# Performance work log

Hardware: AMD Instinct MI355X
Metric: run time of the kernel (lower is better)

Reference implementation:

```python
import jax, jax.numpy as jnp
import numpy as np
from jax import lax
from jax.scipy.special import logsumexp

B, T, H, L = 64, 512, 768, 9


def setup_inputs() -> dict:
    key = jax.random.key(0)
    k1, k2, k3, k4, k5 = jax.random.split(key, 5)
    hidden = jax.random.normal(k1, (B, T, H), dtype=jnp.float32)
    W = jax.random.normal(k2, (L, H), dtype=jnp.float32) * 0.02
    b = jnp.zeros((L,), dtype=jnp.float32)
    transitions = jax.random.normal(k3, (L, L), dtype=jnp.float32) * 0.1
    lengths = jax.random.randint(k4, (B,), T // 2, T + 1)
    seq_mask = jnp.arange(T)[None, :] < lengths[:, None]          # [B,T] bool
    labels = jax.random.randint(k5, (B, T), 0, L).astype(jnp.int32)
    labels = jnp.where(seq_mask, labels, -100).astype(jnp.int32)   # -100 = ignore
    attention_mask = seq_mask.astype(jnp.int32)
    return {"hidden": hidden, "W": W, "b": b, "transitions": transitions,
            "labels": labels, "attention_mask": attention_mask}


def _crf_nll(logits, tags, transitions, mask):
    # numerator: joint score of the gold path (no start/end transitions)
    maskf = mask.astype(logits.dtype)
    emit = jnp.take_along_axis(logits, tags[..., None], axis=2)[..., 0]   # [B,T]
    emit_score = (emit * maskf).sum(-1)
    trans = transitions[tags[:, :-1], tags[:, 1:]]                        # [B,T-1]
    trans_score = (trans * maskf[:, 1:]).sum(-1)
    numerator = emit_score + trans_score
    # denominator: forward algorithm (log-sum-exp recurrence over time)
    def step(alpha, xs):
        logit_t, mask_t = xs                                   # [B,L], [B]
        inner = alpha[:, :, None] + transitions[None, :, :] + logit_t[:, None, :]
        new = logsumexp(inner, axis=1)
        return jnp.where(mask_t[:, None], new, alpha), None
    alpha0 = logits[:, 0]                                      # mask[:,0] assumed True
    alpha, _ = lax.scan(step, alpha0,
                        (jnp.transpose(logits[:, 1:], (1, 0, 2)), mask[:, 1:].T))
    denominator = logsumexp(alpha, axis=-1)
    return -(numerator - denominator).sum()


def _viterbi(logits, transitions, mask):
    num_tags = transitions.shape[0]
    identity_bp = jnp.broadcast_to(jnp.arange(num_tags)[None, :], logits.shape[:1] + (num_tags,))

    def vstep(vscore, xs):
        logit_t, mask_t = xs
        inner = vscore[:, :, None] + transitions[None, :, :]   # [B,L_prev,L_cur]
        bp = jnp.argmax(inner, axis=1)                         # [B,L]
        new = jnp.max(inner, axis=1) + logit_t
        vscore = jnp.where(mask_t[:, None], new, vscore)
        bp = jnp.where(mask_t[:, None], bp, identity_bp)       # carry tag through pad
        return vscore, bp

    vscore0 = logits[:, 0]
    vscore, bps = lax.scan(vstep, vscore0,
                           (jnp.transpose(logits[:, 1:], (1, 0, 2)), mask[:, 1:].T))
    last_tag = jnp.argmax(vscore, axis=-1)                     # [B]

    def btstep(tag, bp_t):
        prev = jnp.take_along_axis(bp_t, tag[:, None], axis=1)[:, 0]
        return prev, tag

    first_tag, tags_rest = lax.scan(btstep, last_tag, bps, reverse=True)  # ys[t]=tag_{t+1}
    return jnp.concatenate([first_tag[:, None], tags_rest.T], axis=1)     # [B,T]


def reference(hidden, W, b, transitions, labels, attention_mask):
    mask = (attention_mask != 0) & (labels != -100)            # create_combined_mask
    logits = jnp.einsum('bth,lh->btl', hidden, W) + b          # classifier (dropout=eval)
    tags = jnp.where(labels == -100, 0, labels)                # adjust_labels_for_crf
    loss = _crf_nll(logits, tags, transitions, mask)           # -log_likelihood (summed)
    vtags = _viterbi(logits, transitions, mask)                # [B,T]
    # pad_predictions: prepend -100, shift right, -100 outside the masked span
    bsz = hidden.shape[0]
    neg = jnp.full((bsz, 1), -100, dtype=jnp.int32)
    shifted = jnp.concatenate([neg, vtags[:, :-1].astype(jnp.int32)], axis=1)
    valid = jnp.concatenate([jnp.zeros((bsz, 1), bool), mask[:, :-1]], axis=1)
    predictions = jnp.where(valid, shifted, -100)
    return loss, predictions
```

## Files before the change

### kernel.cpp

```cpp
#include <hip/hip_runtime.h>

#define BATCH 64
#define TLEN  512
#define HDIM  768
#define LTAGS 9

#define WS_LOGD 0
#define WS_LOGF 2359296
#define WS_VM   3538944
#define WS_AM   6193152
#define WS_NUM  6856704
#define WS_LOSS 6857216

__global__ __launch_bounds__(256) void logits_kernel(
    const float* __restrict__ hidden, const float* __restrict__ W,
    const float* __restrict__ bvec, double* __restrict__ logitsD,
    float* __restrict__ logitsF)
{
    __shared__ float sW[LTAGS * HDIM];
    __shared__ float sb[LTAGS];
    const int tid = threadIdx.x;
    for (int i = tid; i < LTAGS * HDIM; i += 256) sW[i] = W[i];
    if (tid < LTAGS) sb[tid] = bvec[tid];
    __syncthreads();

    const int lane = tid & 63;
    const int wave = tid >> 6;
    const int sub  = lane & 7;
    const int rg   = lane >> 3;

    const int rowBase = blockIdx.x * 64 + wave * 16;
    const int r0 = rowBase + rg;
    const int r1 = rowBase + rg + 8;
    const float* h0p = hidden + (size_t)r0 * HDIM;
    const float* h1p = hidden + (size_t)r1 * HDIM;

    double acc0[LTAGS], acc1[LTAGS];
    #pragma unroll
    for (int l = 0; l < LTAGS; ++l) { acc0[l] = 0.0; acc1[l] = 0.0; }

    #pragma unroll 2
    for (int i = 0; i < 24; ++i) {
        const int off = i * 32 + sub * 4;
        const float4 h0 = *(const float4*)(h0p + off);
        const float4 h1 = *(const float4*)(h1p + off);
        #pragma unroll
        for (int l = 0; l < LTAGS; ++l) {
            const float4 w = *(const float4*)&sW[l * HDIM + off];
            float d0 = h0.x * w.x;
            d0 = fmaf(h0.y, w.y, d0); d0 = fmaf(h0.z, w.z, d0); d0 = fmaf(h0.w, w.w, d0);
            float d1 = h1.x * w.x;
            d1 = fmaf(h1.y, w.y, d1); d1 = fmaf(h1.z, w.z, d1); d1 = fmaf(h1.w, w.w, d1);
            acc0[l] += (double)d0;
            acc1[l] += (double)d1;
        }
    }
    #pragma unroll
    for (int l = 0; l < LTAGS; ++l) {
        double v0 = acc0[l], v1 = acc1[l];
        #pragma unroll
        for (int off = 4; off > 0; off >>= 1) {
            v0 += __shfl_down(v0, off);
            v1 += __shfl_down(v1, off);
        }
        acc0[l] = v0; acc1[l] = v1;
    }
    if (sub == 0) {
        #pragma unroll
        for (int l = 0; l < LTAGS; ++l) {
            double v0 = acc0[l] + (double)sb[l];
            double v1 = acc1[l] + (double)sb[l];
            logitsD[(size_t)r0 * LTAGS + l] = v0;
            logitsD[(size_t)r1 * LTAGS + l] = v1;
            logitsF[(size_t)r0 * LTAGS + l] = (float)v0;
            logitsF[(size_t)r1 * LTAGS + l] = (float)v1;
        }
    }
}

__global__ __launch_bounds__(256) void chunk_kernel(
    const float* __restrict__ trans, const int* __restrict__ labels,
    const int* __restrict__ att, const double* __restrict__ logitsD,
    const float* __restrict__ logitsF,
    double* __restrict__ wsVM, float* __restrict__ wsAM,
    double* __restrict__ wsNum)
{
    __shared__ double sT64[81];
    __shared__ float  sE32[81];
    const int tid = threadIdx.x;
    if (tid < 81) { float tv = trans[tid]; sT64[tid] = (double)tv; sE32[tid] = __expf(tv); }
    __syncthreads();

    const int blk = blockIdx.x;
    if (blk < 144) {
        const int gid = blk * 256 + tid;
        const int b   = gid / 576;
        const int rem = gid - b * 576;
        const int c   = rem / 9;
        const int i   = rem - c * 9;

        double M[LTAGS];
        #pragma unroll
        for (int j = 0; j < LTAGS; ++j) M[j] = (i == j) ? 0.0 : -1e300;

        const double* lrow = logitsD + ((size_t)b * TLEN + (c * 8 + 1)) * LTAGS;
        const int* lab = labels + b * TLEN;
        const int* am  = att + b * TLEN;
        const int t0 = c * 8 + 1;

        double lg[LTAGS], lgN[LTAGS];
        #pragma unroll
        for (int j = 0; j < LTAGS; ++j) lg[j] = lrow[j];
        bool mk = (am[t0] != 0) && (lab[t0] != -100);

        for (int s = 0; s < 8; ++s) {
            bool mkN = false;
            const int tn = t0 + s + 1;
            if (s < 7 && tn <= TLEN - 1) {
                const double* ln = lrow + (s + 1) * LTAGS;
                #pragma unroll
                for (int j = 0; j < LTAGS; ++j) lgN[j] = ln[j];
                mkN = (am[tn] != 0) && (lab[tn] != -100);
            }
            double nw[LTAGS];
            #pragma unroll
            for (int j = 0; j < LTAGS; ++j) {
                double bst = M[0] + sT64[j];
                #pragma unroll
                for (int k = 1; k < LTAGS; ++k) {
                    double cnd = M[k] + sT64[k * LTAGS + j];
                    bst = fmax(bst, cnd);
                }
                nw[j] = bst + lg[j];
            }
            #pragma unroll
            for (int j = 0; j < LTAGS; ++j) { M[j] = mk ? nw[j] : M[j]; lg[j] = lgN[j]; }
            mk = mkN;
        }
        double* dst = wsVM + (((size_t)b * 64 + c) * LTAGS + i) * LTAGS;
        #pragma unroll
        for (int j = 0; j < LTAGS; ++j) dst[j] = M[j];
    } else if (blk < 216) {
        const int gid = (blk - 144) * 256 + tid;
        const int b   = gid / 288;
        const int rem = gid - b * 288;
        const int c   = rem / 9;
        const int i   = rem - c * 9;

        float M[LTAGS];
        #pragma unroll
        for (int j = 0; j < LTAGS; ++j) M[j] = (i == j) ? 0.f : -1e30f;

        const float* lrow = logitsF + ((size_t)b * TLEN + (c * 16 + 1)) * LTAGS;
        const int* lab = labels + b * TLEN;
        const int* am  = att + b * TLEN;
        const int t0 = c * 16 + 1;

        float lg[LTAGS], lgN[LTAGS];
        #pragma unroll
        for (int j = 0; j < LTAGS; ++j) lg[j] = lrow[j];
        bool mk = (am[t0] != 0) && (lab[t0] != -100);

        for (int s = 0; s < 16; ++s) {
            bool mkN = false;
            const int tn = t0 + s + 1;
            if (s < 15 && tn <= TLEN - 1) {
                const float* ln = lrow + (s + 1) * LTAGS;
                #pragma unroll
                for (int j = 0; j < LTAGS; ++j) lgN[j] = ln[j];
                mkN = (am[tn] != 0) && (lab[tn] != -100);
            }
            float m = M[0];
            #pragma unroll
            for (int k = 1; k < LTAGS; ++k) m = fmaxf(m, M[k]);
            float P[LTAGS];
            #pragma unroll
            for (int k = 0; k < LTAGS; ++k) P[k] = __expf(M[k] - m);
            float nw[LTAGS];
            #pragma unroll
            for (int j = 0; j < LTAGS; ++j) {
                float sacc = P[0] * sE32[j];
                #pragma unroll
                for (int k = 1; k < LTAGS; ++k) sacc = fmaf(P[k], sE32[k * LTAGS + j], sacc);
                nw[j] = m + __logf(sacc) + lg[j];
            }
            #pragma unroll
            for (int j = 0; j < LTAGS; ++j) { M[j] = mk ? nw[j] : M[j]; lg[j] = lgN[j]; }
            mk = mkN;
        }
        float* dst = wsAM + (((size_t)b * 32 + c) * LTAGS + i) * LTAGS;
        #pragma unroll
        for (int j = 0; j < LTAGS; ++j) dst[j] = M[j];
    } else {
        const int bb   = (blk - 216) * 4 + (tid >> 6);
        const int lane = tid & 63;
        const int* lab = labels + bb * TLEN;
        const int* am  = att + bb * TLEN;
        const double* lrowb = logitsD + (size_t)bb * TLEN * LTAGS;
        double part = 0.0;
        #pragma unroll
        for (int k = 0; k < 8; ++k) {
            const int t = lane + k * 64;
            int lv = lab[t], av = am[t];
            bool mkc = (av != 0) && (lv != -100);
            int tg = (lv == -100) ? 0 : lv;
            if (mkc) part += lrowb[(size_t)t * LTAGS + tg];
            if (t < TLEN - 1) {
                int lv2 = lab[t + 1], av2 = am[t + 1];
                bool mk2 = (av2 != 0) && (lv2 != -100);
                int tg2 = (lv2 == -100) ? 0 : lv2;
                if (mk2) part += sT64[tg * LTAGS + tg2];
            }
        }
        #pragma unroll
        for (int off = 32; off > 0; off >>= 1) part += __shfl_down(part, off);
        if (lane == 0) wsNum[bb] = part;
    }
}

__global__ __launch_bounds__(128) void crf2_kernel(
    const float* __restrict__ trans, const int* __restrict__ labels,
    const int* __restrict__ att, const double* __restrict__ logitsD,
    const double* __restrict__ wsVM, const float* __restrict__ wsAM,
    const double* __restrict__ wsNum, double* __restrict__ wsLoss,
    float* __restrict__ out)
{
    __shared__ __align__(16) double sVM[64 * 81];
    __shared__ __align__(16) float  sAM[32 * 81];
    __shared__ double sVstart[65 * LTAGS];
    __shared__ unsigned long long sBPp[513];
    __shared__ int sTagB[65];
    __shared__ double sT64[81];
    __shared__ unsigned char sMk[513];
    __shared__ double sDen;
    __shared__ int sLast;

    const int b = blockIdx.x, tid = threadIdx.x;
    const int wave = tid >> 6, lane = tid & 63;
    const unsigned long long IDMAP = 0x876543210ull;

    const double2* gVM = (const double2*)(wsVM + (size_t)b * 64 * 81);
    double2* sVM2 = (double2*)sVM;
    for (int i = tid; i < 2592; i += 128) sVM2[i] = gVM[i];
    const float4* gAM = (const float4*)(wsAM + (size_t)b * 32 * 81);
    float4* sAM4 = (float4*)sAM;
    for (int i = tid; i < 648; i += 128) sAM4[i] = gAM[i];

    const int* lab = labels + b * TLEN;
    const int* am  = att + b * TLEN;
    for (int t = tid; t < TLEN; t += 128) {
        int lv = lab[t], av = am[t];
        sMk[t] = (av != 0 && lv != -100) ? 1 : 0;
    }
    if (tid == 0) sMk[TLEN] = 0;
    if (tid < 81) sT64[tid] = (double)trans[tid];
    __syncthreads();

    if (wave == 0) {
        const int j = (lane < LTAGS) ? lane : (LTAGS - 1);
        double v = logitsD[(size_t)b * TLEN * LTAGS + j];
        double Mc[LTAGS], Mn[LTAGS];
        #pragma unroll
        for (int i = 0; i < LTAGS; ++i) Mc[i] = sVM[i * LTAGS + j];
        for (int c = 0; c < 64; ++c) {
            if (c < 63) {
                #pragma unroll
                for (int i = 0; i < LTAGS; ++i) Mn[i] = sVM[(c + 1) * 81 + i * LTAGS + j];
            }
            if (lane < LTAGS) sVstart[c * LTAGS + j] = v;
            double g[LTAGS];
            #pragma unroll
            for (int i = 0; i < LTAGS; ++i) g[i] = __shfl(v, i);
            double bst = g[0] + Mc[0];
            #pragma unroll
            for (int i = 1; i < LTAGS; ++i) bst = fmax(bst, g[i] + Mc[i]);
            v = bst;
            if (c < 63) {
                #pragma unroll
                for (int i = 0; i < LTAGS; ++i) Mc[i] = Mn[i];
            }
        }
        if (lane < LTAGS) sVstart[64 * LTAGS + j] = v;
        double g[LTAGS];
        #pragma unroll
        for (int i = 0; i < LTAGS; ++i) g[i] = __shfl(v, i);
        if (lane == 0) {
            int bi = 0; double bv = g[0];
            #pragma unroll
            for (int i = 1; i < LTAGS; ++i) if (g[i] > bv) { bv = g[i]; bi = i; }
            sLast = bi;
        }
    } else {
        const int j = (lane < LTAGS) ? lane : (LTAGS - 1);
        float v = (float)logitsD[(size_t)b * TLEN * LTAGS + j];
        float Mc[LTAGS], Mn[LTAGS];
        #pragma unroll
        for (int i = 0; i < LTAGS; ++i) Mc[i] = sAM[i * LTAGS + j];
        for (int c = 0; c < 32; ++c) {
            if (c < 31) {
                #pragma unroll
                for (int i = 0; i < LTAGS; ++i) Mn[i] = sAM[(c + 1) * 81 + i * LTAGS + j];
            }
            float g[LTAGS];
            #pragma unroll
            for (int i = 0; i < LTAGS; ++i) g[i] = __shfl(v, i);
            float a[LTAGS];
            #pragma unroll
            for (int i = 0; i < LTAGS; ++i) a[i] = g[i] + Mc[i];
            float m = a[0];
            #pragma unroll
            for (int i = 1; i < LTAGS; ++i) m = fmaxf(m, a[i]);
            float sacc = 0.f;
            #pragma unroll
            for (int i = 0; i < LTAGS; ++i) sacc += __expf(a[i] - m);
            v = m + __logf(sacc);
            if (c < 31) {
                #pragma unroll
                for (int i = 0; i < LTAGS; ++i) Mc[i] = Mn[i];
            }
        }
        float g[LTAGS];
        #pragma unroll
        for (int i = 0; i < LTAGS; ++i) g[i] = __shfl(v, i);
        if (lane == 0) {
            float m = g[0];
            #pragma unroll
            for (int i = 1; i < LTAGS; ++i) m = fmaxf(m, g[i]);
            float sacc = 0.f;
            #pragma unroll
            for (int i = 0; i < LTAGS; ++i) sacc += __expf(g[i] - m);
            sDen = (double)(m + __logf(sacc));
        }
    }
    __syncthreads();

    unsigned long long S = IDMAP;
    if (tid < 64) {
        const int c = tid;
        double v[LTAGS];
        #pragma unroll
        for (int j = 0; j < LTAGS; ++j) v[j] = sVstart[c * LTAGS + j];
        const double* lrow = logitsD + ((size_t)b * TLEN + (c * 8 + 1)) * LTAGS;
        double lg[LTAGS], lgN[LTAGS];
        #pragma unroll
        for (int j = 0; j < LTAGS; ++j) lg[j] = lrow[j];

        for (int s = 0; s < 8; ++s) {
            const int t = c * 8 + 1 + s;
            if (s < 7 && t + 1 <= TLEN - 1) {
                const double* ln = lrow + (s + 1) * LTAGS;
                #pragma unroll
                for (int j = 0; j < LTAGS; ++j) lgN[j] = ln[j];
            }
            const bool mk = (sMk[t] != 0);
            unsigned long long pk = 0;
            double nv[LTAGS];
            #pragma unroll
            for (int j = 0; j < LTAGS; ++j) {
                double bst = v[0] + sT64[j];
                int bi = 0;
                #pragma unroll
                for (int k = 1; k < LTAGS; ++k) {
                    double cnd = v[k] + sT64[k * LTAGS + j];
                    bool gt = cnd > bst;
                    bst = gt ? cnd : bst;
                    bi  = gt ? k : bi;
                }
                nv[j] = bst + lg[j];
                pk |= ((unsigned long long)bi) << (4 * j);
            }
            pk = mk ? pk : IDMAP;
            sBPp[t] = pk;
            #pragma unroll
            for (int j = 0; j < LTAGS; ++j) { v[j] = mk ? nv[j] : v[j]; lg[j] = lgN[j]; }
        }
        unsigned long long G = IDMAP;
        for (int s = 7; s >= 0; --s) {
            const unsigned long long bp = sBPp[c * 8 + 1 + s];
            unsigned long long ng = 0;
            #pragma unroll
            for (int j = 0; j < LTAGS; ++j) {
                int gj = (int)((G >> (4 * j)) & 15);
                int f  = (int)((bp >> (4 * gj)) & 15);
                ng |= ((unsigned long long)f) << (4 * j);
            }
            G = ng;
        }
        S = G;
    }

    #pragma unroll
    for (int d = 1; d < 64; d <<= 1) {
        unsigned long long Sn = __shfl_down(S, d);
        if (wave == 0 && lane + d < 64) {
            unsigned long long R = 0;
            #pragma unroll
            for (int x = 0; x < LTAGS; ++x) {
                int y = (int)((Sn >> (4 * x)) & 15);
                int z = (int)((S >> (4 * y)) & 15);
                R |= ((unsigned long long)z) << (4 * x);
            }
            S = R;
        }
    }
    if (tid < 64) {
        const int lt = sLast;
        sTagB[tid] = (int)((S >> (4 * lt)) & 15);
        if (tid == 0) sTagB[64] = lt;
    }
    __syncthreads();

    if (tid < 64) {
        const int c = tid;
        int cur = sTagB[c + 1];
        float* po = out + 1 + b * TLEN;
        for (int s = 8; s >= 1; --s) {
            const int t = c * 8 + s;
            if (t < TLEN) {
                int nxt = (int)((sBPp[t] >> (4 * cur)) & 15);
                po[t] = sMk[t - 1] ? (float)nxt : -100.f;
                cur = nxt;
            }
        }
    }
    if (tid == 0) {
        out[1 + b * TLEN] = -100.f;
        wsLoss[b] = sDen - wsNum[b];
    }
}

__global__ __launch_bounds__(64) void loss_kernel(
    const double* __restrict__ wsLoss, float* __restrict__ out)
{
    double v = wsLoss[threadIdx.x];
    #pragma unroll
    for (int off = 32; off > 0; off >>= 1) v += __shfl_down(v, off);
    if (threadIdx.x == 0) out[0] = (float)v;
}

extern "C" void kernel_launch(void* const* d_in, const int* in_sizes, int n_in,
                              void* d_out, int out_size, void* d_ws, size_t ws_size,
                              hipStream_t stream)
{
    const float* hidden = (const float*)d_in[0];
    const float* W      = (const float*)d_in[1];
    const float* bvec   = (const float*)d_in[2];
    const float* trans  = (const float*)d_in[3];
    const int*   labels = (const int*)d_in[4];
    const int*   att    = (const int*)d_in[5];
    float* out = (float*)d_out;

    char* ws = (char*)d_ws;
    double* logitsD = (double*)(ws + WS_LOGD);
    float*  logitsF = (float*)(ws + WS_LOGF);
    double* wsVM    = (double*)(ws + WS_VM);
    float*  wsAM    = (float*)(ws + WS_AM);
    double* wsNum   = (double*)(ws + WS_NUM);
    double* wsLoss  = (double*)(ws + WS_LOSS);

    logits_kernel<<<512, 256, 0, stream>>>(hidden, W, bvec, logitsD, logitsF);
    chunk_kernel<<<232, 256, 0, stream>>>(trans, labels, att, logitsD, logitsF,
                                          wsVM, wsAM, wsNum);
    crf2_kernel<<<BATCH, 128, 0, stream>>>(trans, labels, att, logitsD,
                                           wsVM, wsAM, wsNum, wsLoss, out);
    loss_kernel<<<1, 64, 0, stream>>>(wsLoss, out);
}
```

Measured before the change: 218.6 us.

## Fuse CRF chunk, combine, and loss kernels into one split-block kernel

Merges the chunked max-plus/log-sum-exp matrix kernel, the per-batch combine kernel and the loss reduction into one 128-block kernel. Viterbi and forward-algorithm work for each sequence go to separate blocks, chunk matrices stay in shared memory instead of global workspace, and the last block to finish sums the loss through an atomic ticket. The Viterbi backpointer pass now spreads across 9 lanes per chunk using shuffles, and backpointers are stored as bytes. This removes two kernel launches and the global round trips, at the cost of larger 576-thread blocks, heavier shared memory use, and only 128 blocks to fill the GPU.

```diff
diff --git a/kernel.cpp b/kernel.cpp
--- a/kernel.cpp
+++ b/kernel.cpp
@@ -7,19 +7,18 @@
 
 #define WS_LOGD 0
 #define WS_LOGF 2359296
-#define WS_VM   3538944
-#define WS_AM   6193152
-#define WS_NUM  6856704
-#define WS_LOSS 6857216
+#define WS_LOSS 3538944
+#define WS_CNT  3539456
 
 __global__ __launch_bounds__(256) void logits_kernel(
     const float* __restrict__ hidden, const float* __restrict__ W,
     const float* __restrict__ bvec, double* __restrict__ logitsD,
-    float* __restrict__ logitsF)
+    float* __restrict__ logitsF, unsigned int* __restrict__ wsCnt)
 {
     __shared__ float sW[LTAGS * HDIM];
     __shared__ float sb[LTAGS];
     const int tid = threadIdx.x;
+    if (blockIdx.x == 0 && tid == 0) *wsCnt = 0u;
     for (int i = tid; i < LTAGS * HDIM; i += 256) sW[i] = W[i];
     if (tid < LTAGS) sb[tid] = bvec[tid];
     __syncthreads();
@@ -78,364 +77,333 @@
     }
 }
 
-__global__ __launch_bounds__(256) void chunk_kernel(
+__global__ __launch_bounds__(576) void crf_fused(
     const float* __restrict__ trans, const int* __restrict__ labels,
     const int* __restrict__ att, const double* __restrict__ logitsD,
-    const float* __restrict__ logitsF,
-    double* __restrict__ wsVM, float* __restrict__ wsAM,
-    double* __restrict__ wsNum)
-{
-    __shared__ double sT64[81];
-    __shared__ float  sE32[81];
-    const int tid = threadIdx.x;
-    if (tid < 81) { float tv = trans[tid]; sT64[tid] = (double)tv; sE32[tid] = __expf(tv); }
-    __syncthreads();
-
-    const int blk = blockIdx.x;
-    if (blk < 144) {
-        const int gid = blk * 256 + tid;
-        const int b   = gid / 576;
-        const int rem = gid - b * 576;
-        const int c   = rem / 9;
-        const int i   = rem - c * 9;
-
-        double M[LTAGS];
-        #pragma unroll
-        for (int j = 0; j < LTAGS; ++j) M[j] = (i == j) ? 0.0 : -1e300;
-
-        const double* lrow = logitsD + ((size_t)b * TLEN + (c * 8 + 1)) * LTAGS;
-        const int* lab = labels + b * TLEN;
-        const int* am  = att + b * TLEN;
-        const int t0 = c * 8 + 1;
-
-        double lg[LTAGS], lgN[LTAGS];
-        #pragma unroll
-        for (int j = 0; j < LTAGS; ++j) lg[j] = lrow[j];
-        bool mk = (am[t0] != 0) && (lab[t0] != -100);
-
-        for (int s = 0; s < 8; ++s) {
-            bool mkN = false;
-            const int tn = t0 + s + 1;
-            if (s < 7 && tn <= TLEN - 1) {
-                const double* ln = lrow + (s + 1) * LTAGS;
-                #pragma unroll
-                for (int j = 0; j < LTAGS; ++j) lgN[j] = ln[j];
-                mkN = (am[tn] != 0) && (lab[tn] != -100);
-            }
-            double nw[LTAGS];
-            #pragma unroll
-            for (int j = 0; j < LTAGS; ++j) {
-                double bst = M[0] + sT64[j];
-                #pragma unroll
-                for (int k = 1; k < LTAGS; ++k) {
-                    double cnd = M[k] + sT64[k * LTAGS + j];
-                    bst = fmax(bst, cnd);
-                }
-                nw[j] = bst + lg[j];
-            }
-            #pragma unroll
-            for (int j = 0; j < LTAGS; ++j) { M[j] = mk ? nw[j] : M[j]; lg[j] = lgN[j]; }
-            mk = mkN;
-        }
-        double* dst = wsVM + (((size_t)b * 64 + c) * LTAGS + i) * LTAGS;
-        #pragma unroll
-        for (int j = 0; j < LTAGS; ++j) dst[j] = M[j];
-    } else if (blk < 216) {
-        const int gid = (blk - 144) * 256 + tid;
-        const int b   = gid / 288;
-        const int rem = gid - b * 288;
-        const int c   = rem / 9;
-        const int i   = rem - c * 9;
-
-        float M[LTAGS];
-        #pragma unroll
-        for (int j = 0; j < LTAGS; ++j) M[j] = (i == j) ? 0.f : -1e30f;
-
-        const float* lrow = logitsF + ((size_t)b * TLEN + (c * 16 + 1)) * LTAGS;
-        const int* lab = labels + b * TLEN;
-        const int* am  = att + b * TLEN;
-        const int t0 = c * 16 + 1;
-
-        float lg[LTAGS], lgN[LTAGS];
-        #pragma unroll
-        for (int j = 0; j < LTAGS; ++j) lg[j] = lrow[j];
-        bool mk = (am[t0] != 0) && (lab[t0] != -100);
-
-        for (int s = 0; s < 16; ++s) {
-            bool mkN = false;
-            const int tn = t0 + s + 1;
-            if (s < 15 && tn <= TLEN - 1) {
-                const float* ln = lrow + (s + 1) * LTAGS;
-                #pragma unroll
-                for (int j = 0; j < LTAGS; ++j) lgN[j] = ln[j];
-                mkN = (am[tn] != 0) && (lab[tn] != -100);
-            }
-            float m = M[0];
-            #pragma unroll
-            for (int k = 1; k < LTAGS; ++k) m = fmaxf(m, M[k]);
-            float P[LTAGS];
-            #pragma unroll
-            for (int k = 0; k < LTAGS; ++k) P[k] = __expf(M[k] - m);
-            float nw[LTAGS];
-            #pragma unroll
-            for (int j = 0; j < LTAGS; ++j) {
-                float sacc = P[0] * sE32[j];
-                #pragma unroll
-                for (int k = 1; k < LTAGS; ++k) sacc = fmaf(P[k], sE32[k * LTAGS + j], sacc);
-                nw[j] = m + __logf(sacc) + lg[j];
-            }
-            #pragma unroll
-            for (int j = 0; j < LTAGS; ++j) { M[j] = mk ? nw[j] : M[j]; lg[j] = lgN[j]; }
-            mk = mkN;
-        }
-        float* dst = wsAM + (((size_t)b * 32 + c) * LTAGS + i) * LTAGS;
-        #pragma unroll
-        for (int j = 0; j < LTAGS; ++j) dst[j] = M[j];
-    } else {
-        const int bb   = (blk - 216) * 4 + (tid >> 6);
-        const int lane = tid & 63;
-        const int* lab = labels + bb * TLEN;
-        const int* am  = att + bb * TLEN;
-        const double* lrowb = logitsD + (size_t)bb * TLEN * LTAGS;
-        double part = 0.0;
-        #pragma unroll
-        for (int k = 0; k < 8; ++k) {
-            const int t = lane + k * 64;
-            int lv = lab[t], av = am[t];
-            bool mkc = (av != 0) && (lv != -100);
-            int tg = (lv == -100) ? 0 : lv;
-            if (mkc) part += lrowb[(size_t)t * LTAGS + tg];
-            if (t < TLEN - 1) {
-                int lv2 = lab[t + 1], av2 = am[t + 1];
-                bool mk2 = (av2 != 0) && (lv2 != -100);
-                int tg2 = (lv2 == -100) ? 0 : lv2;
-                if (mk2) part += sT64[tg * LTAGS + tg2];
-            }
-        }
-        #pragma unroll
-        for (int off = 32; off > 0; off >>= 1) part += __shfl_down(part, off);
-        if (lane == 0) wsNum[bb] = part;
-    }
-}
-
-__global__ __launch_bounds__(128) void crf2_kernel(
-    const float* __restrict__ trans, const int* __restrict__ labels,
-    const int* __restrict__ att, const double* __restrict__ logitsD,
-    const double* __restrict__ wsVM, const float* __restrict__ wsAM,
-    const double* __restrict__ wsNum, double* __restrict__ wsLoss,
-    float* __restrict__ out)
+    const float* __restrict__ logitsF, double* __restrict__ wsLoss,
+    unsigned int* __restrict__ wsCnt, float* __restrict__ out)
 {
     __shared__ __align__(16) double sVM[64 * 81];
     __shared__ __align__(16) float  sAM[32 * 81];
     __shared__ double sVstart[65 * LTAGS];
-    __shared__ unsigned long long sBPp[513];
+    __shared__ unsigned char sBPb[513 * 16];
+    __shared__ double sT64[81];
+    __shared__ float  sE32[81];
+    __shared__ unsigned char sMk[TLEN + 1];
     __shared__ int sTagB[65];
-    __shared__ double sT64[81];
-    __shared__ unsigned char sMk[513];
-    __shared__ double sDen;
+    __shared__ double sDen, sNum;
     __shared__ int sLast;
-
-    const int b = blockIdx.x, tid = threadIdx.x;
+    __shared__ unsigned int sTicket;
+
+    const int tid  = threadIdx.x;
     const int wave = tid >> 6, lane = tid & 63;
-    const unsigned long long IDMAP = 0x876543210ull;
-
-    const double2* gVM = (const double2*)(wsVM + (size_t)b * 64 * 81);
-    double2* sVM2 = (double2*)sVM;
-    for (int i = tid; i < 2592; i += 128) sVM2[i] = gVM[i];
-    const float4* gAM = (const float4*)(wsAM + (size_t)b * 32 * 81);
-    float4* sAM4 = (float4*)sAM;
-    for (int i = tid; i < 648; i += 128) sAM4[i] = gAM[i];
-
+    const int blk  = blockIdx.x;
+    const bool isVit = (blk < BATCH);
+    const int b = isVit ? blk : (blk - BATCH);
+
+    if (tid < 81) { float tv = trans[tid]; sT64[tid] = (double)tv; sE32[tid] = __expf(tv); }
     const int* lab = labels + b * TLEN;
     const int* am  = att + b * TLEN;
-    for (int t = tid; t < TLEN; t += 128) {
-        int lv = lab[t], av = am[t];
-        sMk[t] = (av != 0 && lv != -100) ? 1 : 0;
+    for (int t = tid; t < TLEN; t += 576)
+        sMk[t] = (am[t] != 0 && lab[t] != -100) ? 1 : 0;
+    if (tid == 0) sMk[TLEN] = 0;
+    __syncthreads();
+
+    if (isVit) {
+        {
+            const int c = tid / 9;
+            const int i = tid - c * 9;
+            double M[LTAGS];
+            #pragma unroll
+            for (int j = 0; j < LTAGS; ++j) M[j] = (i == j) ? 0.0 : -1e300;
+
+            const double* lrow = logitsD + ((size_t)b * TLEN + (c * 8 + 1)) * LTAGS;
+            const int t0 = c * 8 + 1;
+            double lg[LTAGS], lgN[LTAGS];
+            #pragma unroll
+            for (int j = 0; j < LTAGS; ++j) lg[j] = lrow[j];
+            bool mk = sMk[t0] != 0;
+
+            for (int s = 0; s < 8; ++s) {
+                bool mkN = false;
+                const int tn = t0 + s + 1;
+                if (s < 7 && tn <= TLEN - 1) {
+                    const double* ln = lrow + (s + 1) * LTAGS;
+                    #pragma unroll
+                    for (int j = 0; j < LTAGS; ++j) lgN[j] = ln[j];
+                    mkN = sMk[tn] != 0;
+                }
+                double nw[LTAGS];
+                #pragma unroll
+                for (int j = 0; j < LTAGS; ++j) {
+                    double bst = M[0] + sT64[j];
+                    #pragma unroll
+                    for (int k = 1; k < LTAGS; ++k) {
+                        double cnd = M[k] + sT64[k * LTAGS + j];
+                        bst = fmax(bst, cnd);
+                    }
+                    nw[j] = bst + lg[j];
+                }
+                #pragma unroll
+                for (int j = 0; j < LTAGS; ++j) { M[j] = mk ? nw[j] : M[j]; lg[j] = lgN[j]; }
+                mk = mkN;
+            }
+            double* dst = &sVM[(c * LTAGS + i) * LTAGS];
+            #pragma unroll
+            for (int j = 0; j < LTAGS; ++j) dst[j] = M[j];
+        }
+        __syncthreads();
+
+        if (wave == 0) {
+            const int j = (lane < LTAGS) ? lane : (LTAGS - 1);
+            double v = logitsD[(size_t)b * TLEN * LTAGS + j];
+            double Mc[LTAGS], Mn[LTAGS];
+            #pragma unroll
+            for (int i = 0; i < LTAGS; ++i) Mc[i] = sVM[i * LTAGS + j];
+            for (int c = 0; c < 64; ++c) {
+                if (c < 63) {
+                    #pragma unroll
+                    for (int i = 0; i < LTAGS; ++i) Mn[i] = sVM[(c + 1) * 81 + i * LTAGS + j];
+                }
+                if (lane < LTAGS) sVstart[c * LTAGS + j] = v;
+                double g[LTAGS];
+                #pragma unroll
+                for (int i = 0; i < LTAGS; ++i) g[i] = __shfl(v, i);
+                double bst = g[0] + Mc[0];
+                #pragma unroll
+                for (int i = 1; i < LTAGS; ++i) bst = fmax(bst, g[i] + Mc[i]);
+                v = bst;
+                if (c < 63) {
+                    #pragma unroll
+                    for (int i = 0; i < LTAGS; ++i) Mc[i] = Mn[i];
+                }
+            }
+            if (lane < LTAGS) sVstart[64 * LTAGS + j] = v;
+            double g[LTAGS];
+            #pragma unroll
+            for (int i = 0; i < LTAGS; ++i) g[i] = __shfl(v, i);
+            if (lane == 0) {
+                int bi = 0; double bv = g[0];
+                #pragma unroll
+                for (int i = 1; i < LTAGS; ++i) if (g[i] > bv) { bv = g[i]; bi = i; }
+                sLast = bi;
+            }
+        }
+        __syncthreads();
+
+        {
+            const int grp = tid >> 4;
+            const int lig = tid & 15;
+            const int jr = (lig < 9) ? lig : 8;
+            const int gbase = lane & 48;
+            for (int pass = 0; pass < 2; ++pass) {
+                const int c = pass * 36 + grp;
+                if (c < 64) {
+                    double v = sVstart[c * LTAGS + jr];
+                    const double* lrow = logitsD + ((size_t)b * TLEN + (c * 8 + 1)) * LTAGS;
+                    double lg = lrow[jr];
+                    for (int s = 0; s < 8; ++s) {
+                        const int t = c * 8 + 1 + s;
+                        double lgN = 0.0;
+                        if (s < 7 && t + 1 <= TLEN - 1) lgN = lrow[(s + 1) * LTAGS + jr];
+                        const bool mk = sMk[t] != 0;
+                        double g0 = __shfl(v, gbase + 0);
+                        double bst = g0 + sT64[jr];
+                        int bi = 0;
+                        #pragma unroll
+                        for (int k = 1; k < LTAGS; ++k) {
+                            double gk = __shfl(v, gbase + k);
+                            double cnd = gk + sT64[k * LTAGS + jr];
+                            bool gt = cnd > bst;
+                            bst = gt ? cnd : bst;
+                            bi  = gt ? k : bi;
+                        }
+                        double nv = bst + lg;
+                        int bp = mk ? bi : jr;
+                        if (lig < 9) sBPb[t * 16 + lig] = (unsigned char)bp;
+                        v  = mk ? nv : v;
+                        lg = lgN;
+                    }
+                }
+            }
+        }
+        __syncthreads();
+
+        if (tid < 64) {
+            int Gm[LTAGS];
+            #pragma unroll
+            for (int j = 0; j < LTAGS; ++j) Gm[j] = j;
+            for (int s = 7; s >= 0; --s) {
+                const int t = tid * 8 + 1 + s;
+                #pragma unroll
+                for (int j = 0; j < LTAGS; ++j) Gm[j] = sBPb[t * 16 + Gm[j]];
+            }
+            unsigned long long S = 0;
+            #pragma unroll
+            for (int j = 0; j < LTAGS; ++j) S |= ((unsigned long long)Gm[j]) << (4 * j);
+
+            #pragma unroll
+            for (int d = 1; d < 64; d <<= 1) {
+                unsigned long long Sn = __shfl_down(S, d);
+                if (lane + d < 64) {
+                    unsigned long long R = 0;
+                    #pragma unroll
+                    for (int x = 0; x < LTAGS; ++x) {
+                        int y = (int)((Sn >> (4 * x)) & 15);
+                        int z = (int)((S >> (4 * y)) & 15);
+                        R |= ((unsigned long long)z) << (4 * x);
+                    }
+                    S = R;
+                }
+            }
+            const int lt = sLast;
+            sTagB[tid] = (int)((S >> (4 * lt)) & 15);
+            if (tid == 0) sTagB[64] = lt;
+        }
+        __syncthreads();
+
+        if (tid < 64) {
+            const int c = tid;
+            int cur = sTagB[c + 1];
+            float* po = out + 1 + b * TLEN;
+            for (int s = 8; s >= 1; --s) {
+                const int t = c * 8 + s;
+                if (t < TLEN) {
+                    int nxt = (int)sBPb[t * 16 + cur];
+                    po[t] = sMk[t - 1] ? (float)nxt : -100.f;
+                    cur = nxt;
+                }
+            }
+        }
+        if (tid == 0) out[1 + b * TLEN] = -100.f;
+    } else {
+        if (tid < 288) {
+            const int c = tid / 9;
+            const int i = tid - c * 9;
+            float M[LTAGS];
+            #pragma unroll
+            for (int j = 0; j < LTAGS; ++j) M[j] = (i == j) ? 0.f : -1e30f;
+
+            const float* lrow = logitsF + ((size_t)b * TLEN + (c * 16 + 1)) * LTAGS;
+            const int t0 = c * 16 + 1;
+            float lg[LTAGS], lgN[LTAGS];
+            #pragma unroll
+            for (int j = 0; j < LTAGS; ++j) lg[j] = lrow[j];
+            bool mk = sMk[t0] != 0;
+
+            for (int s = 0; s < 16; ++s) {
+                bool mkN = false;
+                const int tn = t0 + s + 1;
+                if (s < 15 && tn <= TLEN - 1) {
+                    const float* ln = lrow + (s + 1) * LTAGS;
+                    #pragma unroll
+                    for (int j = 0; j < LTAGS; ++j) lgN[j] = ln[j];
+                    mkN = sMk[tn] != 0;
+                }
+                float m = M[0];
+                #pragma unroll
+                for (int k = 1; k < LTAGS; ++k) m = fmaxf(m, M[k]);
+                float P[LTAGS];
+                #pragma unroll
+                for (int k = 0; k < LTAGS; ++k) P[k] = __expf(M[k] - m);
+                float nw[LTAGS];
+                #pragma unroll
+                for (int j = 0; j < LTAGS; ++j) {
+                    float sacc = P[0] * sE32[j];
+                    #pragma unroll
+                    for (int k = 1; k < LTAGS; ++k) sacc = fmaf(P[k], sE32[k * LTAGS + j], sacc);
+                    nw[j] = m + __logf(sacc) + lg[j];
+                }
+                #pragma unroll
+                for (int j = 0; j < LTAGS; ++j) { M[j] = mk ? nw[j] : M[j]; lg[j] = lgN[j]; }
+                mk = mkN;
+            }
+            float* dst = &sAM[(c * LTAGS + i) * LTAGS];
+            #pragma unroll
+            for (int j = 0; j < LTAGS; ++j) dst[j] = M[j];
+        } else if (tid >= 512) {
+            const double* lrowb = logitsD + (size_t)b * TLEN * LTAGS;
+            double part = 0.0;
+            #pragma unroll
+            for (int k = 0; k < 8; ++k) {
+                const int t = lane + k * 64;
+                int lv = lab[t], av = am[t];
+                bool mkc = (av != 0) && (lv != -100);
+                int tg = (lv == -100) ? 0 : lv;
+                if (mkc) part += lrowb[(size_t)t * LTAGS + tg];
+                if (t < TLEN - 1) {
+                    int lv2 = lab[t + 1], av2 = am[t + 1];
+                    bool mk2 = (av2 != 0) && (lv2 != -100);
+                    int tg2 = (lv2 == -100) ? 0 : lv2;
+                    if (mk2) part += sT64[tg * LTAGS + tg2];
+                }
+            }
+            #pragma unroll
+            for (int off = 32; off > 0; off >>= 1) part += __shfl_down(part, off);
+            if (lane == 0) sNum = part;
+        }
+        __syncthreads();
+
+        if (wave == 0) {
+            const int j = (lane < LTAGS) ? lane : (LTAGS - 1);
+            float v = (float)logitsD[(size_t)b * TLEN * LTAGS + j];
+            float Mc[LTAGS], Mn[LTAGS];
+            #pragma unroll
+            for (int i = 0; i < LTAGS; ++i) Mc[i] = sAM[i * LTAGS + j];
+            for (int c = 0; c < 32; ++c) {
+                if (c < 31) {
+                    #pragma unroll
+                    for (int i = 0; i < LTAGS; ++i) Mn[i] = sAM[(c + 1) * 81 + i * LTAGS + j];
+                }
+                float g[LTAGS];
+                #pragma unroll
+                for (int i = 0; i < LTAGS; ++i) g[i] = __shfl(v, i);
+                float a[LTAGS];
+                #pragma unroll
+                for (int i = 0; i < LTAGS; ++i) a[i] = g[i] + Mc[i];
+                float m = a[0];
+                #pragma unroll
+                for (int i = 1; i < LTAGS; ++i) m = fmaxf(m, a[i]);
+                float sacc = 0.f;
+                #pragma unroll
+                for (int i = 0; i < LTAGS; ++i) sacc += __expf(a[i] - m);
+                v = m + __logf(sacc);
+                if (c < 31) {
+                    #pragma unroll
+                    for (int i = 0; i < LTAGS; ++i) Mc[i] = Mn[i];
+                }
+            }
+            float g[LTAGS];
+            #pragma unroll
+            for (int i = 0; i < LTAGS; ++i) g[i] = __shfl(v, i);
+            if (lane == 0) {
+                float m = g[0];
+                #pragma unroll
+                for (int i = 1; i < LTAGS; ++i) m = fmaxf(m, g[i]);
+                float sacc = 0.f;
+                #pragma unroll
+                for (int i = 0; i < LTAGS; ++i) sacc += __expf(g[i] - m);
+                sDen = (double)(m + __logf(sacc));
+            }
+        }
+        __syncthreads();
+
+        if (tid == 0) {
+            wsLoss[b] = sDen - sNum;
+            __threadfence();
+            sTicket = atomicAdd(wsCnt, 1u);
+        }
+        __syncthreads();
+        if (sTicket == (BATCH - 1)) {
+            __threadfence();
+            if (tid < 64) {
+                double v = wsLoss[tid];
+                #pragma unroll
+                for (int off = 32; off > 0; off >>= 1) v += __shfl_down(v, off);
+                if (tid == 0) out[0] = (float)v;
+            }
+        }
     }
-    if (tid == 0) sMk[TLEN] = 0;
-    if (tid < 81) sT64[tid] = (double)trans[tid];
-    __syncthreads();
-
-    if (wave == 0) {
-        const int j = (lane < LTAGS) ? lane : (LTAGS - 1);
-        double v = logitsD[(size_t)b * TLEN * LTAGS + j];
-        double Mc[LTAGS], Mn[LTAGS];
-        #pragma unroll
-        for (int i = 0; i < LTAGS; ++i) Mc[i] = sVM[i * LTAGS + j];
-        for (int c = 0; c < 64; ++c) {
-            if (c < 63) {
-                #pragma unroll
-                for (int i = 0; i < LTAGS; ++i) Mn[i] = sVM[(c + 1) * 81 + i * LTAGS + j];
-            }
-            if (lane < LTAGS) sVstart[c * LTAGS + j] = v;
-            double g[LTAGS];
-            #pragma unroll
-            for (int i = 0; i < LTAGS; ++i) g[i] = __shfl(v, i);
-            double bst = g[0] + Mc[0];
-            #pragma unroll
-            for (int i = 1; i < LTAGS; ++i) bst = fmax(bst, g[i] + Mc[i]);
-            v = bst;
-            if (c < 63) {
-                #pragma unroll
-                for (int i = 0; i < LTAGS; ++i) Mc[i] = Mn[i];
-            }
-        }
-        if (lane < LTAGS) sVstart[64 * LTAGS + j] = v;
-        double g[LTAGS];
-        #pragma unroll
-        for (int i = 0; i < LTAGS; ++i) g[i] = __shfl(v, i);
-        if (lane == 0) {
-            int bi = 0; double bv = g[0];
-            #pragma unroll
-            for (int i = 1; i < LTAGS; ++i) if (g[i] > bv) { bv = g[i]; bi = i; }
-            sLast = bi;
-        }
-    } else {
-        const int j = (lane < LTAGS) ? lane : (LTAGS - 1);
-        float v = (float)logitsD[(size_t)b * TLEN * LTAGS + j];
-        float Mc[LTAGS], Mn[LTAGS];
-        #pragma unroll
-        for (int i = 0; i < LTAGS; ++i) Mc[i] = sAM[i * LTAGS + j];
-        for (int c = 0; c < 32; ++c) {
-            if (c < 31) {
-                #pragma unroll
-                for (int i = 0; i < LTAGS; ++i) Mn[i] = sAM[(c + 1) * 81 + i * LTAGS + j];
-            }
-            float g[LTAGS];
-            #pragma unroll
-            for (int i = 0; i < LTAGS; ++i) g[i] = __shfl(v, i);
-            float a[LTAGS];
-            #pragma unroll
-            for (int i = 0; i < LTAGS; ++i) a[i] = g[i] + Mc[i];
-            float m = a[0];
-            #pragma unroll
-            for (int i = 1; i < LTAGS; ++i) m = fmaxf(m, a[i]);
-            float sacc = 0.f;
-            #pragma unroll
-            for (int i = 0; i < LTAGS; ++i) sacc += __expf(a[i] - m);
-            v = m + __logf(sacc);
-            if (c < 31) {
-                #pragma unroll
-                for (int i = 0; i < LTAGS; ++i) Mc[i] = Mn[i];
-            }
-        }
-        float g[LTAGS];
-        #pragma unroll
-        for (int i = 0; i < LTAGS; ++i) g[i] = __shfl(v, i);
-        if (lane == 0) {
-            float m = g[0];
-            #pragma unroll
-            for (int i = 1; i < LTAGS; ++i) m = fmaxf(m, g[i]);
-            float sacc = 0.f;
-            #pragma unroll
-            for (int i = 0; i < LTAGS; ++i) sacc += __expf(g[i] - m);
-            sDen = (double)(m + __logf(sacc));
-        }
-    }
-    __syncthreads();
-
-    unsigned long long S = IDMAP;
-    if (tid < 64) {
-        const int c = tid;
-        double v[LTAGS];
-        #pragma unroll
-        for (int j = 0; j < LTAGS; ++j) v[j] = sVstart[c * LTAGS + j];
-        const double* lrow = logitsD + ((size_t)b * TLEN + (c * 8 + 1)) * LTAGS;
-        double lg[LTAGS], lgN[LTAGS];
-        #pragma unroll
-        for (int j = 0; j < LTAGS; ++j) lg[j] = lrow[j];
-
-        for (int s = 0; s < 8; ++s) {
-            const int t = c * 8 + 1 + s;
-            if (s < 7 && t + 1 <= TLEN - 1) {
-                const double* ln = lrow + (s + 1) * LTAGS;
-                #pragma unroll
-                for (int j = 0; j < LTAGS; ++j) lgN[j] = ln[j];
-            }
-            const bool mk = (sMk[t] != 0);
-            unsigned long long pk = 0;
-            double nv[LTAGS];
-            #pragma unroll
-            for (int j = 0; j < LTAGS; ++j) {
-                double bst = v[0] + sT64[j];
-                int bi = 0;
-                #pragma unroll
-                for (int k = 1; k < LTAGS; ++k) {
-                    double cnd = v[k] + sT64[k * LTAGS + j];
-                    bool gt = cnd > bst;
-                    bst = gt ? cnd : bst;
-                    bi  = gt ? k : bi;
-                }
-                nv[j] = bst + lg[j];
-                pk |= ((unsigned long long)bi) << (4 * j);
-            }
-            pk = mk ? pk : IDMAP;
-            sBPp[t] = pk;
-            #pragma unroll
-            for (int j = 0; j < LTAGS; ++j) { v[j] = mk ? nv[j] : v[j]; lg[j] = lgN[j]; }
-        }
-        unsigned long long G = IDMAP;
-        for (int s = 7; s >= 0; --s) {
-            const unsigned long long bp = sBPp[c * 8 + 1 + s];
-            unsigned long long ng = 0;
-            #pragma unroll
-            for (int j = 0; j < LTAGS; ++j) {
-                int gj = (int)((G >> (4 * j)) & 15);
-                int f  = (int)((bp >> (4 * gj)) & 15);
-                ng |= ((unsigned long long)f) << (4 * j);
-            }
-            G = ng;
-        }
-        S = G;
-    }
-
-    #pragma unroll
-    for (int d = 1; d < 64; d <<= 1) {
-        unsigned long long Sn = __shfl_down(S, d);
-        if (wave == 0 && lane + d < 64) {
-            unsigned long long R = 0;
-            #pragma unroll
-            for (int x = 0; x < LTAGS; ++x) {
-                int y = (int)((Sn >> (4 * x)) & 15);
-                int z = (int)((S >> (4 * y)) & 15);
-                R |= ((unsigned long long)z) << (4 * x);
-            }
-            S = R;
-        }
-    }
-    if (tid < 64) {
-        const int lt = sLast;
-        sTagB[tid] = (int)((S >> (4 * lt)) & 15);
-        if (tid == 0) sTagB[64] = lt;
-    }
-    __syncthreads();
-
-    if (tid < 64) {
-        const int c = tid;
-        int cur = sTagB[c + 1];
-        float* po = out + 1 + b * TLEN;
-        for (int s = 8; s >= 1; --s) {
-            const int t = c * 8 + s;
-            if (t < TLEN) {
-                int nxt = (int)((sBPp[t] >> (4 * cur)) & 15);
-                po[t] = sMk[t - 1] ? (float)nxt : -100.f;
-                cur = nxt;
-            }
-        }
-    }
-    if (tid == 0) {
-        out[1 + b * TLEN] = -100.f;
-        wsLoss[b] = sDen - wsNum[b];
-    }
-}
-
-__global__ __launch_bounds__(64) void loss_kernel(
-    const double* __restrict__ wsLoss, float* __restrict__ out)
-{
-    double v = wsLoss[threadIdx.x];
-    #pragma unroll
-    for (int off = 32; off > 0; off >>= 1) v += __shfl_down(v, off);
-    if (threadIdx.x == 0) out[0] = (float)v;
 }
 
 extern "C" void kernel_launch(void* const* d_in, const int* in_sizes, int n_in,
@@ -453,15 +421,10 @@
     char* ws = (char*)d_ws;
     double* logitsD = (double*)(ws + WS_LOGD);
     float*  logitsF = (float*)(ws + WS_LOGF);
-    double* wsVM    = (double*)(ws + WS_VM);
-    float*  wsAM    = (float*)(ws + WS_AM);
-    double* wsNum   = (double*)(ws + WS_NUM);
     double* wsLoss  = (double*)(ws + WS_LOSS);
-
-    logits_kernel<<<512, 256, 0, stream>>>(hidden, W, bvec, logitsD, logitsF);
-    chunk_kernel<<<232, 256, 0, stream>>>(trans, labels, att, logitsD, logitsF,
-                                          wsVM, wsAM, wsNum);
-    crf2_kernel<<<BATCH, 128, 0, stream>>>(trans, labels, att, logitsD,
-                                           wsVM, wsAM, wsNum, wsLoss, out);
-    loss_kernel<<<1, 64, 0, stream>>>(wsLoss, out);
+    unsigned int* wsCnt = (unsigned int*)(ws + WS_CNT);
+
+    logits_kernel<<<512, 256, 0, stream>>>(hidden, W, bvec, logitsD, logitsF, wsCnt);
+    crf_fused<<<2 * BATCH, 576, 0, stream>>>(trans, labels, att, logitsD, logitsF,
+                                             wsLoss, wsCnt, out);
 }
```

New measurement: 247.0 us. +12.9%, slower.
